# Optimization experiments

Hardware: AMD Instinct MI355X
Metric: run time of the kernel (lower is better)

## Reference

```python
import jax, jax.numpy as jnp
import numpy as np

HEADS = 8
DIM_HEAD = 64
DIM = 512
MAX_POS_EMB = 512
SCALE = DIM_HEAD ** -0.5


def setup_inputs() -> dict:
    key = jax.random.key(0)
    ks = jax.random.split(key, 6)
    B, N = 2, 2048
    inner = HEADS * DIM_HEAD  # 512
    x = jax.random.normal(ks[0], (B, N, DIM), dtype=jnp.float32)
    # torch Linear weights stored as [out, in]; we keep [in, out] for x @ W
    Wq = jax.random.normal(ks[1], (DIM, inner), dtype=jnp.float32) * (DIM ** -0.5)
    Wkv = jax.random.normal(ks[2], (DIM, 2 * inner), dtype=jnp.float32) * (DIM ** -0.5)
    Wo = jax.random.normal(ks[3], (inner, DIM), dtype=jnp.float32) * (inner ** -0.5)
    bo = jax.random.normal(ks[4], (DIM,), dtype=jnp.float32) * 0.02
    rel_emb = jax.random.normal(ks[5], (2 * MAX_POS_EMB + 1, DIM_HEAD), dtype=jnp.float32)
    return {"x": x, "Wq": Wq, "Wkv": Wkv, "Wo": Wo, "bo": bo, "rel_emb": rel_emb}


def reference(x, Wq, Wkv, Wo, bo, rel_emb):
    B, N, _ = x.shape
    h, d = HEADS, DIM_HEAD
    q = x @ Wq                                # [B, N, h*d]
    kv = x @ Wkv                              # [B, N, 2*h*d]
    k, v = jnp.split(kv, 2, axis=-1)
    to_heads = lambda t: t.reshape(B, N, h, d).transpose(0, 2, 1, 3)  # [B, h, N, d]
    q, k, v = to_heads(q), to_heads(k), to_heads(v)

    dots = jnp.einsum('bhid,bhjd->bhij', q, k) * SCALE  # [B, h, N, N]

    # relative positional bias: dist clamped to [-max, max], shifted to [0, 2*max]
    seq = jnp.arange(N)
    dist = jnp.clip(seq[:, None] - seq[None, :], -MAX_POS_EMB, MAX_POS_EMB) + MAX_POS_EMB
    rel = rel_emb[dist]                                 # [N, N, d]
    pos_attn = jnp.einsum('bhnd,njd->bhnj', q, rel) * SCALE
    dots = dots + pos_attn

    attn = jax.nn.softmax(dots, axis=-1)
    out = jnp.einsum('bhij,bhjd->bhid', attn, v)        # [B, h, N, d]
    out = out.transpose(0, 2, 1, 3).reshape(B, N, h * d)
    return out @ Wo + bo
```

## Files before the change

### kernel.cpp

```cpp
#include <hip/hip_runtime.h>
#include <hip/hip_bf16.h>
#include <stdint.h>

#define HEADS 8
#define DHEAD 64
#define DIM 512
#define NSEQ 2048
#define BATCH 2
#define NROWS (BATCH * NSEQ)
#define QKV_N 1536
#define REL_ROWS 1025
#define REL_PITCH_ROWS 1088
#define NSPLIT 2
#define KV_PER_SPLIT (NSEQ / NSPLIT)

static constexpr float SCALE_LOG2E = 0.125f * 1.4426950408889634f;

typedef __attribute__((ext_vector_type(8))) short bf16x8;
typedef __attribute__((ext_vector_type(4))) float f32x4;

__device__ __forceinline__ uint16_t f2bf(float f) {
    union { float f; uint32_t u; } v{f};
    uint32_t r = (v.u + 0x7FFFu + ((v.u >> 16) & 1u)) >> 16;
    return (uint16_t)r;
}

__global__ void prep_misc(const float* __restrict__ x, const float* __restrict__ rel,
                          uint16_t* __restrict__ xb, uint16_t* __restrict__ relb) {
    int total = NROWS * DIM + REL_PITCH_ROWS * DHEAD;
    for (int idx = blockIdx.x * blockDim.x + threadIdx.x; idx < total; idx += gridDim.x * blockDim.x) {
        if (idx < NROWS * DIM) {
            xb[idx] = f2bf(x[idx]);
        } else {
            int i2 = idx - NROWS * DIM;
            relb[i2] = (i2 < REL_ROWS * DHEAD) ? f2bf(rel[i2]) : (uint16_t)0;
        }
    }
}

__global__ void prep_w(const float* __restrict__ Wq, const float* __restrict__ Wkv,
                       const float* __restrict__ Wo,
                       uint16_t* __restrict__ Wqkv_t, uint16_t* __restrict__ Wo_t) {
    __shared__ float tile[32][33];
    int bid = blockIdx.x;
    const float* src; uint16_t* dst; int J, ti, tj;
    if (bid < 256)      { src = Wq;  dst = Wqkv_t;             J = 512;  ti = bid >> 4;        tj = bid & 15; }
    else if (bid < 768) { int b = bid - 256; src = Wkv; dst = Wqkv_t + 512 * 512; J = 1024; ti = b >> 5; tj = b & 31; }
    else                { int b = bid - 768; src = Wo;  dst = Wo_t;   J = 512;  ti = b >> 4;        tj = b & 15; }
    int tx = threadIdx.x & 31, ty = threadIdx.x >> 5;
    int k0 = ti * 32, j0 = tj * 32;
    #pragma unroll
    for (int i = 0; i < 4; i++) tile[ty + 8 * i][tx] = src[(size_t)(k0 + ty + 8 * i) * J + j0 + tx];
    __syncthreads();
    #pragma unroll
    for (int i = 0; i < 4; i++) dst[(size_t)(j0 + ty + 8 * i) * 512 + k0 + tx] = f2bf(tile[tx][ty + 8 * i]);
}

template <bool BF16_OUT>
__global__ __launch_bounds__(256) void gemm128(const uint16_t* __restrict__ A,
                                               const uint16_t* __restrict__ Bt,
                                               void* __restrict__ Cout,
                                               const float* __restrict__ bias,
                                               int K, int ldc) {
    __shared__ char lds[32768];
    char* ldsA = lds;
    char* ldsB = lds + 16384;
    int m0 = blockIdx.x * 128, n0 = blockIdx.y * 128;
    int t = threadIdx.x, lane = t & 63, w = t >> 6;
    int wr = w >> 1, wc = w & 1;
    int l15 = lane & 15, lh = lane >> 4;
    f32x4 acc[4][4] = {};
    for (int k0 = 0; k0 < K; k0 += 64) {
        __syncthreads();
        {
            int row = t >> 3, ch = t & 7;
            #pragma unroll
            for (int p = 0; p < 4; p++) {
                int r = row + 32 * p;
                bf16x8 va = *(const bf16x8*)(A + (size_t)(m0 + r) * K + k0 + ch * 8);
                *(bf16x8*)(ldsA + r * 128 + ((ch * 16) ^ ((r & 7) << 4))) = va;
                bf16x8 vb = *(const bf16x8*)(Bt + (size_t)(n0 + r) * K + k0 + ch * 8);
                *(bf16x8*)(ldsB + r * 128 + ((ch * 16) ^ ((r & 7) << 4))) = vb;
            }
        }
        __syncthreads();
        #pragma unroll
        for (int kk = 0; kk < 2; kk++) {
            bf16x8 a[4], b[4];
            #pragma unroll
            for (int mi = 0; mi < 4; mi++) {
                int m = wr * 64 + mi * 16 + l15;
                a[mi] = *(const bf16x8*)(ldsA + m * 128 + ((kk * 64 + lh * 16) ^ ((m & 7) << 4)));
            }
            #pragma unroll
            for (int ni = 0; ni < 4; ni++) {
                int n = wc * 64 + ni * 16 + l15;
                b[ni] = *(const bf16x8*)(ldsB + n * 128 + ((kk * 64 + lh * 16) ^ ((n & 7) << 4)));
            }
            #pragma unroll
            for (int mi = 0; mi < 4; mi++)
                #pragma unroll
                for (int ni = 0; ni < 4; ni++)
                    acc[mi][ni] = __builtin_amdgcn_mfma_f32_16x16x32_bf16(a[mi], b[ni], acc[mi][ni], 0, 0, 0);
        }
    }
    #pragma unroll
    for (int mi = 0; mi < 4; mi++)
        #pragma unroll
        for (int ni = 0; ni < 4; ni++)
            #pragma unroll
            for (int i = 0; i < 4; i++) {
                int m = m0 + wr * 64 + mi * 16 + lh * 4 + i;
                int n = n0 + wc * 64 + ni * 16 + l15;
                float v = acc[mi][ni][i];
                if constexpr (BF16_OUT) ((uint16_t*)Cout)[(size_t)m * ldc + n] = f2bf(v);
                else                    ((float*)Cout)[(size_t)m * ldc + n] = v + bias[n];
            }
}

__global__ __launch_bounds__(512, 4) void attn_kernel(const uint16_t* __restrict__ QKV,
                                                      const uint16_t* __restrict__ relb,
                                                      float* __restrict__ Opart,
                                                      float* __restrict__ mlpart) {
    __shared__ char lds[53248];
    char* ldsQ = lds;
    char* ldsKV = lds + 16384;

    int flat = blockIdx.x + 16 * (blockIdx.y + 8 * blockIdx.z);
    int x = (flat & 7) * 64 + (flat >> 3);
    int qb = x & 15, h = (x >> 4) & 7, z = x >> 7;
    int b = z >> 1, sp = z & 1;

    int t = threadIdx.x, lane = t & 63, w = t >> 6;
    int l15 = lane & 15, lh = lane >> 4;
    int row = t >> 3, ch = t & 7;
    int n0 = qb * 128;
    int kvbase = sp * KV_PER_SPLIT;
    size_t rowQ = (size_t)b * NSEQ + n0;

    {
        int buf = t >> 8, idx = t & 255;
        uint32_t val = (idx < 16) ? 0x3F803F80u : 0u;
        char* p = ldsKV + buf * 18432 + 8192 + 8192 + (idx >> 4) * 128 + (idx & 15) * 8;
        *(uint32_t*)(p) = val;
        *(uint32_t*)(p + 4) = val;
    }

    #pragma unroll
    for (int p = 0; p < 2; p++) {
        int r = row + 64 * p;
        bf16x8 v = *(const bf16x8*)(QKV + (rowQ + r) * QKV_N + h * 64 + ch * 8);
        *(bf16x8*)(ldsQ + r * 128 + ((ch * 16) ^ ((r & 7) << 4))) = v;
    }
    __syncthreads();
    bf16x8 qf[2];
    #pragma unroll
    for (int kk = 0; kk < 2; kk++) {
        int m = w * 16 + l15;
        qf[kk] = *(const bf16x8*)(ldsQ + m * 128 + ((kk * 64 + lh * 16) ^ ((m & 7) << 4)));
    }
    char* myP = ldsQ + w * 2048;

    f32x4 biasLo = {}, biasHi = {};
    {
        bf16x8 bl0 = *(const bf16x8*)(relb + lh * 8);
        bf16x8 bl1 = *(const bf16x8*)(relb + lh * 8 + 32);
        bf16x8 bh0 = *(const bf16x8*)(relb + 1024 * 64 + lh * 8);
        bf16x8 bh1 = *(const bf16x8*)(relb + 1024 * 64 + lh * 8 + 32);
        biasLo = __builtin_amdgcn_mfma_f32_16x16x32_bf16(qf[0], bl0, biasLo, 0, 0, 0);
        biasLo = __builtin_amdgcn_mfma_f32_16x16x32_bf16(qf[1], bl1, biasLo, 0, 0, 0);
        biasHi = __builtin_amdgcn_mfma_f32_16x16x32_bf16(qf[0], bh0, biasHi, 0, 0, 0);
        biasHi = __builtin_amdgcn_mfma_f32_16x16x32_bf16(qf[1], bh1, biasHi, 0, 0, 0);
    }

    f32x4 oacc[5] = {};
    float mrow[4];
    #pragma unroll
    for (int i = 0; i < 4; i++) mrow[i] = -INFINITY;

    int exAddr[4];
    #pragma unroll
    for (int i = 0; i < 4; i++)
        exAddr[i] = (((lane & 48) | ((lh * 4 + i + 15 - l15) & 15)) << 2);

    auto load_kv = [&](int tile, bf16x8& kr, bf16x8& vr) {
        size_t gro = ((size_t)b * NSEQ + kvbase + tile * 64 + row) * QKV_N + h * 64 + ch * 8;
        kr = *(const bf16x8*)(QKV + gro + 512);
        vr = *(const bf16x8*)(QKV + gro + 1024);
    };
    auto scatter_kv = [&](int tile, bf16x8& kr, bf16x8& vr) {
        char* ldsK = ldsKV + (tile & 1) * 18432;
        char* ldsV = ldsK + 8192;
        *(bf16x8*)(ldsK + row * 128 + ((ch * 16) ^ ((row & 7) << 4))) = kr;
        #pragma unroll
        for (int dd = 0; dd < 8; dd++) {
            int d = ch * 8 + dd;
            int s = dd ^ ch;
            *(uint16_t*)(ldsV + d * 128 + 2 * (row ^ (s << 3))) = (uint16_t)vr[dd];
        }
    };

    const int NT = KV_PER_SPLIT / 64;
    bf16x8 kr, vr;
    load_kv(0, kr, vr);
    scatter_kv(0, kr, vr);

    #pragma unroll 1
    for (int tt = 0; tt < NT; ++tt) {
        char* ldsK = ldsKV + (tt & 1) * 18432;
        char* ldsV = ldsK + 8192;
        __syncthreads();
        bool pf = (tt + 1 < NT);
        if (pf) load_kv(tt + 1, kr, vr);

        int nk = n0 + w * 16 - (kvbase + tt * 64);
        bool fullLo = (nk <= -527), fullHi = (nk >= 575);

        f32x4 sacc[4] = {};
        __builtin_amdgcn_s_setprio(1);
        #pragma unroll
        for (int kk = 0; kk < 2; kk++)
            #pragma unroll
            for (int nf = 0; nf < 4; nf++) {
                int n = nf * 16 + l15;
                bf16x8 kfv = *(const bf16x8*)(ldsK + n * 128 + ((kk * 64 + lh * 16) ^ ((n & 7) << 4)));
                sacc[nf] = __builtin_amdgcn_mfma_f32_16x16x32_bf16(qf[kk], kfv, sacc[nf], 0, 0, 0);
            }
        __builtin_amdgcn_s_setprio(0);

        if (fullLo || fullHi) {
            f32x4 bc = fullLo ? biasLo : biasHi;
            #pragma unroll
            for (int nf = 0; nf < 4; nf++)
                #pragma unroll
                for (int i = 0; i < 4; i++)
                    sacc[nf][i] += bc[i];
        } else {
            int dlo = nk - 63;
            bf16x8 rfr[2][2];
            {
                int d = dlo + l15;
                d = d < -512 ? -512 : (d > 512 ? 512 : d);
                const uint16_t* rp = relb + (d + 512) * 64 + lh * 8;
                rfr[0][0] = *(const bf16x8*)(rp);
                rfr[0][1] = *(const bf16x8*)(rp + 32);
            }
            f32x4 rect[5] = {};
            #pragma unroll
            for (int f = 0; f < 5; f++) {
                if (f + 1 < 5) {
                    int d = dlo + (f + 1) * 16 + l15;
                    d = d < -512 ? -512 : (d > 512 ? 512 : d);
                    const uint16_t* rp = relb + (d + 512) * 64 + lh * 8;
                    rfr[(f + 1) & 1][0] = *(const bf16x8*)(rp);
                    rfr[(f + 1) & 1][1] = *(const bf16x8*)(rp + 32);
                }
                rect[f] = __builtin_amdgcn_mfma_f32_16x16x32_bf16(qf[0], rfr[f & 1][0], rect[f], 0, 0, 0);
                rect[f] = __builtin_amdgcn_mfma_f32_16x16x32_bf16(qf[1], rfr[f & 1][1], rect[f], 0, 0, 0);
                __builtin_amdgcn_sched_barrier(0);
            }
            #pragma unroll
            for (int i = 0; i < 4; i++) {
                bool hi = (l15 < lh * 4 + i);
                #pragma unroll
                for (int nf = 0; nf < 4; nf++) {
                    float v = hi ? rect[4 - nf][i] : rect[3 - nf][i];
                    union { float f; int s; } un{v};
                    un.s = __builtin_amdgcn_ds_bpermute(exAddr[i], un.s);
                    sacc[nf][i] += un.f;
                }
            }
        }

        float lmax = sacc[0][0];
        #pragma unroll
        for (int nf = 0; nf < 4; nf++)
            #pragma unroll
            for (int i = 0; i < 4; i++) lmax = fmaxf(lmax, sacc[nf][i]);
        float mmin = fminf(fminf(mrow[0], mrow[1]), fminf(mrow[2], mrow[3]));
        if (!__all(lmax <= mmin + 64.0f)) {
            #pragma unroll
            for (int i = 0; i < 4; i++) {
                float mx = fmaxf(fmaxf(sacc[0][i], sacc[1][i]), fmaxf(sacc[2][i], sacc[3][i]));
                mx = fmaxf(mx, __shfl_xor(mx, 1));
                mx = fmaxf(mx, __shfl_xor(mx, 2));
                mx = fmaxf(mx, __shfl_xor(mx, 4));
                mx = fmaxf(mx, __shfl_xor(mx, 8));
                float mnew = fmaxf(mrow[i], mx);
                float alpha = exp2f((mrow[i] - mnew) * SCALE_LOG2E);
                mrow[i] = mnew;
                #pragma unroll
                for (int nf = 0; nf < 5; nf++) oacc[nf][i] *= alpha;
            }
        }

        #pragma unroll
        for (int i = 0; i < 4; i++) {
            int r = lh * 4 + i;
            int rsw = (r & 7) << 4;
            #pragma unroll
            for (int nf = 0; nf < 4; nf++) {
                float p = exp2f((sacc[nf][i] - mrow[i]) * SCALE_LOG2E);
                uint32_t pb;
                asm("v_cvt_pk_bf16_f32 %0, %1, %2" : "=v"(pb) : "v"(p), "v"(p));
                *(uint16_t*)(myP + r * 128 + (((nf * 16 + l15) * 2) ^ rsw)) = (uint16_t)pb;
            }
        }

        asm volatile("s_waitcnt lgkmcnt(0)" ::: "memory");
        __builtin_amdgcn_sched_barrier(0);
        __builtin_amdgcn_s_setprio(1);
        #pragma unroll
        for (int kk = 0; kk < 2; kk++) {
            bf16x8 pa = *(const bf16x8*)(myP + l15 * 128 + ((kk * 64 + lh * 16) ^ ((l15 & 7) << 4)));
            #pragma unroll
            for (int nf = 0; nf < 5; nf++) {
                int d = nf * 16 + l15;
                int sd = (d & 7) ^ ((d >> 3) & 7);
                bf16x8 vb = *(const bf16x8*)(ldsV + d * 128 + 16 * ((kk * 4 + lh) ^ sd));
                oacc[nf] = __builtin_amdgcn_mfma_f32_16x16x32_bf16(pa, vb, oacc[nf], 0, 0, 0);
            }
        }
        __builtin_amdgcn_s_setprio(0);

        if (pf) scatter_kv(tt + 1, kr, vr);
    }

    size_t rbase = ((size_t)(sp * BATCH + b) * HEADS + h) * NSEQ;
    #pragma unroll
    for (int nf = 0; nf < 4; nf++)
        #pragma unroll
        for (int i = 0; i < 4; i++) {
            int r = n0 + w * 16 + lh * 4 + i;
            Opart[(rbase + r) * 64 + nf * 16 + l15] = oacc[nf][i];
        }
    if (l15 == 0) {
        #pragma unroll
        for (int i = 0; i < 4; i++) {
            int r = n0 + w * 16 + lh * 4 + i;
            mlpart[(rbase + r) * 2]     = mrow[i];
            mlpart[(rbase + r) * 2 + 1] = oacc[4][i];
        }
    }
}

__global__ __launch_bounds__(256) void combine_kernel(const float* __restrict__ Opart,
                                                      const float* __restrict__ mlpart,
                                                      uint16_t* __restrict__ attO) {
    int lane = threadIdx.x & 63;
    int R = blockIdx.x * 4 + (threadIdx.x >> 6);
    const int SPSTRIDE = BATCH * HEADS * NSEQ;
    float m1 = mlpart[(size_t)R * 2], l1 = mlpart[(size_t)R * 2 + 1];
    float m2 = mlpart[((size_t)SPSTRIDE + R) * 2], l2 = mlpart[((size_t)SPSTRIDE + R) * 2 + 1];
    float M = fmaxf(m1, m2);
    float w1 = exp2f((m1 - M) * SCALE_LOG2E);
    float w2 = exp2f((m2 - M) * SCALE_LOG2E);
    float Linv = 1.f / (l1 * w1 + l2 * w2);
    float o1 = Opart[(size_t)R * 64 + lane];
    float o2 = Opart[((size_t)SPSTRIDE + R) * 64 + lane];
    float o = (o1 * w1 + o2 * w2) * Linv;
    int bh = R >> 11, n = R & 2047;
    int b = bh >> 3, hh = bh & 7;
    attO[((size_t)(b * NSEQ + n)) * DIM + hh * 64 + lane] = f2bf(o);
}

extern "C" void kernel_launch(void* const* d_in, const int* in_sizes, int n_in,
                              void* d_out, int out_size, void* d_ws, size_t ws_size,
                              hipStream_t stream) {
    const float* x   = (const float*)d_in[0];
    const float* Wq  = (const float*)d_in[1];
    const float* Wkv = (const float*)d_in[2];
    const float* Wo  = (const float*)d_in[3];
    const float* bo  = (const float*)d_in[4];
    const float* rel = (const float*)d_in[5];
    char* ws = (char*)d_ws;
    float*    mlp    = (float*)(ws);
    uint16_t* Wo_t   = (uint16_t*)(ws + 524288);
    uint16_t* relb   = (uint16_t*)(ws + 1048576);
    uint16_t* attO   = (uint16_t*)(ws + 1310720);
    uint16_t* QKV    = (uint16_t*)(ws + 5505024);
    float*    Opart  = (float*)(ws + 18087936);
    uint16_t* Xb     = (uint16_t*)(ws + 18087936);
    uint16_t* Wqkv_t = (uint16_t*)(ws + 22282240);

    prep_misc<<<2048, 256, 0, stream>>>(x, rel, Xb, relb);
    prep_w<<<1024, 256, 0, stream>>>(Wq, Wkv, Wo, Wqkv_t, Wo_t);
    gemm128<true><<<dim3(32, 12), 256, 0, stream>>>(Xb, Wqkv_t, QKV, nullptr, 512, QKV_N);
    attn_kernel<<<dim3(16, 8, 4), 512, 0, stream>>>(QKV, relb, Opart, mlp);
    combine_kernel<<<8192, 256, 0, stream>>>(Opart, mlp, attO);
    gemm128<false><<<dim3(32, 4), 256, 0, stream>>>(attO, Wo_t, (float*)d_out, bo, 512, DIM);
}
```

Before: 132.4 us.

## Stage Q and K tiles via direct global-to-LDS loads and merge prep kernels

Q and K tiles now go straight from global memory into LDS with `global_load_lds`. The XOR swizzle moves to the global source address, so these tiles no longer pass through registers. V still takes the register path so it can be transposed before the scatter. The loop gains an extra barrier at the end of each iteration to protect the double buffer from the asynchronous K writes. The two prep kernels are fused into one launch to drop a launch gap. The extra per-iteration barrier could offset the register and VGPR savings.

```diff
diff --git a/kernel.cpp b/kernel.cpp
--- a/kernel.cpp
+++ b/kernel.cpp
@@ -25,24 +25,25 @@
     return (uint16_t)r;
 }
 
-__global__ void prep_misc(const float* __restrict__ x, const float* __restrict__ rel,
-                          uint16_t* __restrict__ xb, uint16_t* __restrict__ relb) {
-    int total = NROWS * DIM + REL_PITCH_ROWS * DHEAD;
-    for (int idx = blockIdx.x * blockDim.x + threadIdx.x; idx < total; idx += gridDim.x * blockDim.x) {
-        if (idx < NROWS * DIM) {
-            xb[idx] = f2bf(x[idx]);
-        } else {
-            int i2 = idx - NROWS * DIM;
-            relb[i2] = (i2 < REL_ROWS * DHEAD) ? f2bf(rel[i2]) : (uint16_t)0;
-        }
-    }
-}
-
-__global__ void prep_w(const float* __restrict__ Wq, const float* __restrict__ Wkv,
-                       const float* __restrict__ Wo,
-                       uint16_t* __restrict__ Wqkv_t, uint16_t* __restrict__ Wo_t) {
+__global__ void prep_all(const float* __restrict__ x, const float* __restrict__ rel,
+                         const float* __restrict__ Wq, const float* __restrict__ Wkv,
+                         const float* __restrict__ Wo,
+                         uint16_t* __restrict__ xb, uint16_t* __restrict__ relb,
+                         uint16_t* __restrict__ Wqkv_t, uint16_t* __restrict__ Wo_t) {
+    if (blockIdx.x < 2048) {
+        int total = NROWS * DIM + REL_PITCH_ROWS * DHEAD;
+        for (int idx = blockIdx.x * blockDim.x + threadIdx.x; idx < total; idx += 2048 * blockDim.x) {
+            if (idx < NROWS * DIM) {
+                xb[idx] = f2bf(x[idx]);
+            } else {
+                int i2 = idx - NROWS * DIM;
+                relb[i2] = (i2 < REL_ROWS * DHEAD) ? f2bf(rel[i2]) : (uint16_t)0;
+            }
+        }
+        return;
+    }
     __shared__ float tile[32][33];
-    int bid = blockIdx.x;
+    int bid = blockIdx.x - 2048;
     const float* src; uint16_t* dst; int J, ti, tj;
     if (bid < 256)      { src = Wq;  dst = Wqkv_t;             J = 512;  ti = bid >> 4;        tj = bid & 15; }
     else if (bid < 768) { int b = bid - 256; src = Wkv; dst = Wqkv_t + 512 * 512; J = 1024; ti = b >> 5; tj = b & 31; }
@@ -122,7 +123,7 @@
                                                       const uint16_t* __restrict__ relb,
                                                       float* __restrict__ Opart,
                                                       float* __restrict__ mlpart) {
-    __shared__ char lds[53248];
+    __shared__ __align__(16) char lds[53248];
     char* ldsQ = lds;
     char* ldsKV = lds + 16384;
 
@@ -138,6 +139,16 @@
     int kvbase = sp * KV_PER_SPLIT;
     size_t rowQ = (size_t)b * NSEQ + n0;
 
+    int swzSrc = (ch * 16) ^ ((row & 7) << 4);
+
+    #pragma unroll
+    for (int p = 0; p < 2; p++) {
+        int r = row + 64 * p;
+        const char* gsrc = (const char*)(QKV + (rowQ + r) * QKV_N + h * 64)
+                           + ((ch * 16) ^ ((r & 7) << 4));
+        __builtin_amdgcn_global_load_lds(gsrc, ldsQ + p * 8192 + t * 16, 16, 0, 0);
+    }
+
     {
         int buf = t >> 8, idx = t & 255;
         uint32_t val = (idx < 16) ? 0x3F803F80u : 0u;
@@ -146,13 +157,31 @@
         *(uint32_t*)(p + 4) = val;
     }
 
-    #pragma unroll
-    for (int p = 0; p < 2; p++) {
-        int r = row + 64 * p;
-        bf16x8 v = *(const bf16x8*)(QKV + (rowQ + r) * QKV_N + h * 64 + ch * 8);
-        *(bf16x8*)(ldsQ + r * 128 + ((ch * 16) ^ ((r & 7) << 4))) = v;
-    }
+    auto stage_k = [&](int tile) {
+        const char* gsrc = (const char*)(QKV + ((size_t)b * NSEQ + kvbase + tile * 64 + row) * QKV_N
+                                         + 512 + h * 64) + swzSrc;
+        __builtin_amdgcn_global_load_lds(gsrc, ldsKV + (tile & 1) * 18432 + t * 16, 16, 0, 0);
+    };
+    auto load_v = [&](int tile, bf16x8& vr) {
+        vr = *(const bf16x8*)(QKV + ((size_t)b * NSEQ + kvbase + tile * 64 + row) * QKV_N
+                              + 1024 + h * 64 + ch * 8);
+    };
+    auto scatter_v = [&](int tile, bf16x8& vr) {
+        char* ldsV = ldsKV + (tile & 1) * 18432 + 8192;
+        #pragma unroll
+        for (int dd = 0; dd < 8; dd++) {
+            int d = ch * 8 + dd;
+            int s = dd ^ ch;
+            *(uint16_t*)(ldsV + d * 128 + 2 * (row ^ (s << 3))) = (uint16_t)vr[dd];
+        }
+    };
+
+    bf16x8 vr;
+    stage_k(0);
+    load_v(0, vr);
+    scatter_v(0, vr);
     __syncthreads();
+
     bf16x8 qf[2];
     #pragma unroll
     for (int kk = 0; kk < 2; kk++) {
@@ -183,35 +212,18 @@
     for (int i = 0; i < 4; i++)
         exAddr[i] = (((lane & 48) | ((lh * 4 + i + 15 - l15) & 15)) << 2);
 
-    auto load_kv = [&](int tile, bf16x8& kr, bf16x8& vr) {
-        size_t gro = ((size_t)b * NSEQ + kvbase + tile * 64 + row) * QKV_N + h * 64 + ch * 8;
-        kr = *(const bf16x8*)(QKV + gro + 512);
-        vr = *(const bf16x8*)(QKV + gro + 1024);
-    };
-    auto scatter_kv = [&](int tile, bf16x8& kr, bf16x8& vr) {
-        char* ldsK = ldsKV + (tile & 1) * 18432;
-        char* ldsV = ldsK + 8192;
-        *(bf16x8*)(ldsK + row * 128 + ((ch * 16) ^ ((row & 7) << 4))) = kr;
-        #pragma unroll
-        for (int dd = 0; dd < 8; dd++) {
-            int d = ch * 8 + dd;
-            int s = dd ^ ch;
-            *(uint16_t*)(ldsV + d * 128 + 2 * (row ^ (s << 3))) = (uint16_t)vr[dd];
-        }
-    };
-
     const int NT = KV_PER_SPLIT / 64;
-    bf16x8 kr, vr;
-    load_kv(0, kr, vr);
-    scatter_kv(0, kr, vr);
 
     #pragma unroll 1
     for (int tt = 0; tt < NT; ++tt) {
         char* ldsK = ldsKV + (tt & 1) * 18432;
         char* ldsV = ldsK + 8192;
-        __syncthreads();
+        if (tt > 0) __syncthreads();
         bool pf = (tt + 1 < NT);
-        if (pf) load_kv(tt + 1, kr, vr);
+        if (pf) {
+            stage_k(tt + 1);
+            load_v(tt + 1, vr);
+        }
 
         int nk = n0 + w * 16 - (kvbase + tt * 64);
         bool fullLo = (nk <= -527), fullHi = (nk >= 575);
@@ -323,7 +335,8 @@
         }
         __builtin_amdgcn_s_setprio(0);
 
-        if (pf) scatter_kv(tt + 1, kr, vr);
+        if (pf) scatter_v(tt + 1, vr);
+        __syncthreads();
     }
 
     size_t rbase = ((size_t)(sp * BATCH + b) * HEADS + h) * NSEQ;
@@ -383,8 +396,7 @@
     uint16_t* Xb     = (uint16_t*)(ws + 18087936);
     uint16_t* Wqkv_t = (uint16_t*)(ws + 22282240);
 
-    prep_misc<<<2048, 256, 0, stream>>>(x, rel, Xb, relb);
-    prep_w<<<1024, 256, 0, stream>>>(Wq, Wkv, Wo, Wqkv_t, Wo_t);
+    prep_all<<<3072, 256, 0, stream>>>(x, rel, Wq, Wkv, Wo, Xb, relb, Wqkv_t, Wo_t);
     gemm128<true><<<dim3(32, 12), 256, 0, stream>>>(Xb, Wqkv_t, QKV, nullptr, 512, QKV_N);
     attn_kernel<<<dim3(16, 8, 4), 512, 0, stream>>>(QKV, relb, Opart, mlp);
     combine_kernel<<<8192, 256, 0, stream>>>(Opart, mlp, attO);
```

Measured after the change: 134.0 us. No clear change (+1.2%).
